# Kernel tuning notes

Measured on AMD Instinct MI355X. Metric: run time of the kernel, lower is better.

The kernel has to match this reference:

```python
import jax, jax.numpy as jnp
import numpy as np

N = 100000   # nodes
E = 1_600_000  # edges (avg degree 16)
D = 64       # input_dim = hidden_dim = output_dim
EPS = 1e-5   # BatchNorm eps


def setup_inputs() -> dict:
    key = jax.random.key(0)
    ks = jax.random.split(key, 8)
    x = jax.random.normal(ks[0], (N, D), jnp.float32)
    edge_index = jax.random.randint(ks[1], (2, E), 0, N, jnp.int32)

    def lin_w(k, din, dout):
        s = 1.0 / np.sqrt(din)
        return jax.random.uniform(k, (din, dout), jnp.float32, -s, s)

    return {
        "x": x, "edge_index": edge_index,
        "W1": lin_w(ks[2], D, D), "b1": jnp.zeros((D,), jnp.float32),
        "g1": jnp.ones((D,), jnp.float32), "be1": jnp.zeros((D,), jnp.float32),
        "W2": lin_w(ks[3], D, D), "b2": jnp.zeros((D,), jnp.float32),
        "g2": jnp.ones((D,), jnp.float32), "be2": jnp.zeros((D,), jnp.float32),
        "W3": lin_w(ks[4], D, D), "b3": jnp.zeros((D,), jnp.float32),
        "g3": jnp.ones((D,), jnp.float32), "be3": jnp.zeros((D,), jnp.float32),
    }


def gcn_conv(x, src, dst, W, b):
    # GCNConv: out = D^{-1/2}(A+I)D^{-1/2} (x @ W) + b
    n = x.shape[0]
    loops = jnp.arange(n, dtype=src.dtype)
    s = jnp.concatenate([src, loops])  # add self-loops
    d = jnp.concatenate([dst, loops])
    deg = jax.ops.segment_sum(jnp.ones_like(s, jnp.float32), d, num_segments=n)
    dinv = jax.lax.rsqrt(jnp.maximum(deg, 1.0))  # deg >= 1 (self-loops)
    norm = dinv[s] * dinv[d]                     # [E+N]
    xw = x @ W                                   # [N, D]
    msgs = xw[s] * norm[:, None]                 # [E+N, D] gather
    return jax.ops.segment_sum(msgs, d, num_segments=n) + b  # scatter-add


def batch_norm(z, g, be):
    # training-mode BatchNorm1d: batch statistics, biased variance
    mu = jnp.mean(z, axis=0)
    var = jnp.mean(jnp.square(z - mu), axis=0)
    return (z - mu) * jax.lax.rsqrt(var + EPS) * g + be


def reference(x, edge_index, W1, b1, g1, be1, W2, b2, g2, be2, W3, b3, g3, be3):
    src, dst = edge_index[0], edge_index[1]
    z = jax.nn.relu(batch_norm(gcn_conv(x, src, dst, W1, b1), g1, be1))
    z = jax.nn.relu(batch_norm(gcn_conv(z, src, dst, W2, b2), g2, be2))
    z = batch_norm(gcn_conv(z, src, dst, W3, b3), g3, be3)
    # dropout (p=0.1) is identity in eval mode; normalize=False default
    return z
```

## Files before the change

### kernel.cpp

```cpp
#include <hip/hip_runtime.h>

typedef unsigned short ushort_t;
typedef unsigned int uint_t;
typedef float f32x4 __attribute__((ext_vector_type(4)));
typedef short bf16x8 __attribute__((ext_vector_type(8)));

#define NB_AGG 2560
#define BSHIFT 7
#define BROWS 128
#define BCAP 4096
#define NCHUNK 256
#define ZP 72

__device__ __forceinline__ float bf2f_lo(uint_t u) {
    union { uint_t i; float f; } v; v.i = u << 16; return v.f;
}
__device__ __forceinline__ float bf2f_hi(uint_t u) {
    union { uint_t i; float f; } v; v.i = u & 0xffff0000u; return v.f;
}
__device__ __forceinline__ ushort_t f2bf(float f) {
    union { float f; uint_t i; } v; v.f = f;
    uint_t u = v.i;
    uint_t r = (u + 0x7fffu + ((u >> 16) & 1u)) >> 16;
    return (ushort_t)r;
}

__global__ __launch_bounds__(256) void hist2_k(const int* __restrict__ dst,
                                               int* __restrict__ H, int E, int nb) {
    __shared__ int h[1024];
    int b = blockIdx.x, t = threadIdx.x;
    for (int i = t; i < nb; i += 256) h[i] = 0;
    __syncthreads();
    int per = (E + NCHUNK - 1) / NCHUNK;
    int lo = b * per, hi = min(E, lo + per);
    for (int e = lo + t; e < hi; e += 256)
        atomicAdd(&h[dst[e] >> BSHIFT], 1);
    __syncthreads();
    for (int i = t; i < nb; i += 256) H[(size_t)i * NCHUNK + b] = h[i];
}

__global__ __launch_bounds__(256) void scanA_k(const int* __restrict__ v,
                                               int* __restrict__ segsum, int total) {
    int base = blockIdx.x * 1024 + threadIdx.x;
    int s = 0;
#pragma unroll
    for (int i = 0; i < 4; ++i) {
        int idx = base + i * 256;
        if (idx < total) s += v[idx];
    }
    __shared__ int sh[256];
    sh[threadIdx.x] = s;
    __syncthreads();
    for (int off = 128; off > 0; off >>= 1) {
        if (threadIdx.x < off) sh[threadIdx.x] += sh[threadIdx.x + off];
        __syncthreads();
    }
    if (threadIdx.x == 0) segsum[blockIdx.x] = sh[0];
}

__global__ void scanB_k(int* segsum, int nseg) {
    __shared__ int sh[256];
    int t = threadIdx.x;
    int own = (t < nseg) ? segsum[t] : 0;
    sh[t] = own;
    __syncthreads();
    for (int off = 1; off < 256; off <<= 1) {
        int v = (t >= off) ? sh[t - off] : 0;
        __syncthreads();
        sh[t] += v;
        __syncthreads();
    }
    if (t < nseg) segsum[t] = sh[t] - own;
}

__global__ __launch_bounds__(256) void scanC2_k(int* __restrict__ H,
                                                const int* __restrict__ segsum,
                                                int total) {
    int t = threadIdx.x;
    int base = blockIdx.x * 1024 + t * 4;
    int c0 = 0, c1 = 0, c2 = 0, c3 = 0;
    if (base + 0 < total) c0 = H[base + 0];
    if (base + 1 < total) c1 = H[base + 1];
    if (base + 2 < total) c2 = H[base + 2];
    if (base + 3 < total) c3 = H[base + 3];
    int tsum = c0 + c1 + c2 + c3;
    __shared__ int sh[256];
    sh[t] = tsum;
    __syncthreads();
    for (int off = 1; off < 256; off <<= 1) {
        int v = (t >= off) ? sh[t - off] : 0;
        __syncthreads();
        sh[t] += v;
        __syncthreads();
    }
    int excl = segsum[blockIdx.x] + sh[t] - tsum;
    if (base + 0 < total) H[base + 0] = excl;
    if (base + 1 < total) H[base + 1] = excl + c0;
    if (base + 2 < total) H[base + 2] = excl + c0 + c1;
    if (base + 3 < total) H[base + 3] = excl + c0 + c1 + c2;
}

__global__ __launch_bounds__(256) void scat2_k(const int* __restrict__ src,
                                               const int* __restrict__ dst,
                                               const int* __restrict__ H,
                                               int* __restrict__ colA, int E, int nb) {
    __shared__ int cur[1024];
    int b = blockIdx.x, t = threadIdx.x;
    for (int i = t; i < nb; i += 256) cur[i] = H[(size_t)i * NCHUNK + b];
    __syncthreads();
    int per = (E + NCHUNK - 1) / NCHUNK;
    int lo = b * per, hi = min(E, lo + per);
    for (int e = lo + t; e < hi; e += 256) {
        int d = dst[e];
        int bk = d >> BSHIFT;
        int pos = atomicAdd(&cur[bk], 1);
        colA[pos] = (src[e] << BSHIFT) | (d & (BROWS - 1));
    }
}

__global__ __launch_bounds__(256) void build_k(int* __restrict__ colA,
                                               const int* __restrict__ H,
                                               float* __restrict__ dinv,
                                               int* __restrict__ rowp,
                                               int N, int E, int nb) {
    __shared__ int recs[BCAP];
    __shared__ int cnt[BROWS], pfx[BROWS], cur[BROWS];
    int b = blockIdx.x, t = threadIdx.x;
    int base = H[(size_t)b * NCHUNK];
    int next = (b + 1 < nb) ? H[(size_t)(b + 1) * NCHUNK] : E;
    int size = next - base;
    if (size > BCAP) size = BCAP;
    int row0 = b << BSHIFT;

    if (t < BROWS) { cnt[t] = 0; cur[t] = 0; }
    __syncthreads();

    for (int i = t; i < size; i += 256) {
        int r = colA[base + i];
        recs[i] = r;
        atomicAdd(&cnt[r & (BROWS - 1)], 1);
    }
    __syncthreads();

    if (t < BROWS) pfx[t] = cnt[t];
    __syncthreads();
    for (int off = 1; off < BROWS; off <<= 1) {
        int u = 0;
        if (t < BROWS && t >= off) u = pfx[t - off];
        __syncthreads();
        if (t < BROWS) pfx[t] += u;
        __syncthreads();
    }
    if (t < BROWS) {
        int row = row0 + t;
        if (row < N) {
            int ex = pfx[t] - cnt[t];
            rowp[row] = base + ex;
            dinv[row] = rsqrtf((float)cnt[t] + 1.0f);
            if (row == N - 1) rowp[N] = base + pfx[t];
        }
    }
    __syncthreads();

    for (int i = t; i < size; i += 256) {
        int r = recs[i];
        int l = r & (BROWS - 1);
        int pos = base + (pfx[l] - cnt[l]) + atomicAdd(&cur[l], 1);
        colA[pos] = r >> BSHIFT;
    }
}

template <int MODE>
__global__ __launch_bounds__(256) void gemm_k(const float* __restrict__ Zf,
                                              const uint2* __restrict__ Zb,
                                              const float* __restrict__ W,
                                              const float* __restrict__ dinv,
                                              const float* __restrict__ cA,
                                              const float* __restrict__ cC,
                                              ushort_t* __restrict__ XW, int N) {
    __shared__ ushort_t WbT[64 * ZP];
    __shared__ ushort_t Zt[64 * ZP];
    __shared__ ushort_t Ot[4][16 * ZP];
    __shared__ float Al[64], Cl[64], Dl[64];
    int t = threadIdx.x;
    int row0 = blockIdx.x * 64;

    if (t < 64) {
        int r = row0 + t;
        Dl[t] = (r < N) ? dinv[r] : 0.0f;
        if (MODE) { Al[t] = cA[t]; Cl[t] = cC[t]; }
    }
    {
        int col = t & 63, kg = t >> 6;
#pragma unroll
        for (int kk = 0; kk < 16; ++kk) {
            int k = kg * 16 + kk;
            WbT[col * ZP + k] = f2bf(W[k * 64 + col]);
        }
    }
    __syncthreads();

    {
        int r = t >> 2, cg = t & 3;
        int grow = row0 + r;
        bool gv = grow < N;
#pragma unroll
        for (int q = 0; q < 4; ++q) {
            float4 v;
            if (MODE) {
                uint2 p2 = {0, 0};
                if (gv) p2 = Zb[(size_t)grow * 16 + cg * 4 + q];
                v.x = bf2f_lo(p2.x); v.y = bf2f_hi(p2.x);
                v.z = bf2f_lo(p2.y); v.w = bf2f_hi(p2.y);
                int k = cg * 16 + q * 4;
                v.x = fmaxf(Al[k + 0] * v.x + Cl[k + 0], 0.0f);
                v.y = fmaxf(Al[k + 1] * v.y + Cl[k + 1], 0.0f);
                v.z = fmaxf(Al[k + 2] * v.z + Cl[k + 2], 0.0f);
                v.w = fmaxf(Al[k + 3] * v.w + Cl[k + 3], 0.0f);
            } else {
                if (gv) v = *(const float4*)(Zf + (size_t)grow * 64 + cg * 16 + q * 4);
                else { v.x = v.y = v.z = v.w = 0.0f; }
            }
            uint2 p;
            p.x = (uint_t)f2bf(v.x) | ((uint_t)f2bf(v.y) << 16);
            p.y = (uint_t)f2bf(v.z) | ((uint_t)f2bf(v.w) << 16);
            *(uint2*)&Zt[r * ZP + cg * 16 + q * 4] = p;
        }
    }
    __syncthreads();

    int wv = t >> 6, lane = t & 63;
    int mrow = lane & 15;
    int kgrp = lane >> 4;

    f32x4 acc0 = {0, 0, 0, 0}, acc1 = {0, 0, 0, 0};
    f32x4 acc2 = {0, 0, 0, 0}, acc3 = {0, 0, 0, 0};
#pragma unroll
    for (int ks = 0; ks < 2; ++ks) {
        bf16x8 a = *(bf16x8*)&Zt[(wv * 16 + mrow) * ZP + ks * 32 + kgrp * 8];
        bf16x8 b0 = *(bf16x8*)&WbT[(0 + mrow) * ZP + ks * 32 + kgrp * 8];
        bf16x8 b1 = *(bf16x8*)&WbT[(16 + mrow) * ZP + ks * 32 + kgrp * 8];
        bf16x8 b2 = *(bf16x8*)&WbT[(32 + mrow) * ZP + ks * 32 + kgrp * 8];
        bf16x8 b3 = *(bf16x8*)&WbT[(48 + mrow) * ZP + ks * 32 + kgrp * 8];
        acc0 = __builtin_amdgcn_mfma_f32_16x16x32_bf16(a, b0, acc0, 0, 0, 0);
        acc1 = __builtin_amdgcn_mfma_f32_16x16x32_bf16(a, b1, acc1, 0, 0, 0);
        acc2 = __builtin_amdgcn_mfma_f32_16x16x32_bf16(a, b2, acc2, 0, 0, 0);
        acc3 = __builtin_amdgcn_mfma_f32_16x16x32_bf16(a, b3, acc3, 0, 0, 0);
    }

#pragma unroll
    for (int r = 0; r < 4; ++r) {
        int orow = kgrp * 4 + r;
        float dn = Dl[wv * 16 + orow];
        Ot[wv][orow * ZP + 0 + mrow]  = f2bf(acc0[r] * dn);
        Ot[wv][orow * ZP + 16 + mrow] = f2bf(acc1[r] * dn);
        Ot[wv][orow * ZP + 32 + mrow] = f2bf(acc2[r] * dn);
        Ot[wv][orow * ZP + 48 + mrow] = f2bf(acc3[r] * dn);
    }
#pragma unroll
    for (int i = 0; i < 2; ++i) {
        int cid = lane * 2 + i;
        int orow = cid >> 3, seg = cid & 7;
        int grow = row0 + wv * 16 + orow;
        if (grow < N)
            *(uint4*)(XW + (size_t)grow * 64 + seg * 8) =
                *(uint4*)&Ot[wv][orow * ZP + seg * 8];
    }
}

template <int WBF16>
__global__ __launch_bounds__(256) void agg_k(const ushort_t* __restrict__ y,
                                             const int* __restrict__ row_ptr,
                                             const int* __restrict__ colA,
                                             const float* __restrict__ dinv,
                                             float* __restrict__ OUTF,
                                             uint2* __restrict__ OUTB,
                                             float* __restrict__ pS,
                                             float* __restrict__ pQ, int N) {
    __shared__ float ssum[64], ssq[64];
    int t = threadIdx.x, lane = t & 63, wv = t >> 6;
    int rs = lane >> 5;
    int g = (lane >> 4) & 1;
    int c = lane & 15;
    if (t < 64) ssum[t] = 0.0f;
    else if (t < 128) ssq[t - 64] = 0.0f;
    __syncthreads();

    const uint2* y2 = (const uint2*)y;
    float ps0 = 0, ps1 = 0, ps2 = 0, ps3 = 0;
    float pq0 = 0, pq1 = 0, pq2 = 0, pq3 = 0;

    int npair = (N + 1) >> 1;
    for (int p = blockIdx.x * 4 + wv; p < npair; p += NB_AGG * 4) {
        int row = p * 2 + rs;
        bool rv = row < N;
        int rc = rv ? row : N - 1;
        int start = row_ptr[rc];
        int end = row_ptr[rc + 1];
        int len = rv ? (end - start) : 0;
        int ml = max(len, __shfl_xor(len, 32));

        float a0 = 0, a1 = 0, a2 = 0, a3 = 0;
        for (int off = 0; off < ml; off += 16) {
            int sA[8];
            uint_t mA[8];
#pragma unroll
            for (int u = 0; u < 8; ++u) {
                int slot = off + u * 2 + g;
                bool val = slot < len;
                int ec = val ? (start + slot) : 0;
                sA[u] = colA[ec];
                mA[u] = val ? 0xffffffffu : 0u;
            }
#pragma unroll
            for (int u = 0; u < 8; ++u) {
                uint2 v = y2[(size_t)sA[u] * 16 + c];
                v.x &= mA[u]; v.y &= mA[u];
                a0 += bf2f_lo(v.x);
                a1 += bf2f_hi(v.x);
                a2 += bf2f_lo(v.y);
                a3 += bf2f_hi(v.y);
            }
        }

        a0 += __shfl_xor(a0, 16);
        a1 += __shfl_xor(a1, 16);
        a2 += __shfl_xor(a2, 16);
        a3 += __shfl_xor(a3, 16);

        if (g == 0 && rv) {
            float dn = dinv[row];
            uint2 sv = y2[(size_t)row * 16 + c];
            float v0 = dn * (a0 + bf2f_lo(sv.x));
            float v1 = dn * (a1 + bf2f_hi(sv.x));
            float v2 = dn * (a2 + bf2f_lo(sv.y));
            float v3 = dn * (a3 + bf2f_hi(sv.y));
            if (WBF16) {
                uint2 pk;
                pk.x = (uint_t)f2bf(v0) | ((uint_t)f2bf(v1) << 16);
                pk.y = (uint_t)f2bf(v2) | ((uint_t)f2bf(v3) << 16);
                OUTB[(size_t)row * 16 + c] = pk;
            } else {
                float4 o; o.x = v0; o.y = v1; o.z = v2; o.w = v3;
                *(float4*)(OUTF + (size_t)row * 64 + c * 4) = o;
            }
            ps0 += v0; ps1 += v1; ps2 += v2; ps3 += v3;
            pq0 += v0 * v0; pq1 += v1 * v1; pq2 += v2 * v2; pq3 += v3 * v3;
        }
    }

    if (g == 0) {
        atomicAdd(&ssum[c * 4 + 0], ps0); atomicAdd(&ssq[c * 4 + 0], pq0);
        atomicAdd(&ssum[c * 4 + 1], ps1); atomicAdd(&ssq[c * 4 + 1], pq1);
        atomicAdd(&ssum[c * 4 + 2], ps2); atomicAdd(&ssq[c * 4 + 2], pq2);
        atomicAdd(&ssum[c * 4 + 3], ps3); atomicAdd(&ssq[c * 4 + 3], pq3);
    }
    __syncthreads();
    if (t < 64) pS[(size_t)t * NB_AGG + blockIdx.x] = ssum[t];
    else if (t < 128) pQ[(size_t)(t - 64) * NB_AGG + blockIdx.x] = ssq[t - 64];
}

__global__ __launch_bounds__(256) void stats_k(const float* __restrict__ pS,
                                               const float* __restrict__ pQ,
                                               const float* __restrict__ g,
                                               const float* __restrict__ be,
                                               float* __restrict__ cA,
                                               float* __restrict__ cC, int N) {
    int c = blockIdx.x, t = threadIdx.x;
    float s = 0.0f, q = 0.0f;
    for (int i = t; i < NB_AGG; i += 256) {
        s += pS[(size_t)c * NB_AGG + i];
        q += pQ[(size_t)c * NB_AGG + i];
    }
    __shared__ float rs[256], rq[256];
    rs[t] = s; rq[t] = q;
    __syncthreads();
    for (int off = 128; off > 0; off >>= 1) {
        if (t < off) { rs[t] += rs[t + off]; rq[t] += rq[t + off]; }
        __syncthreads();
    }
    if (t == 0) {
        float mu = rs[0] / (float)N;
        float var = rq[0] / (float)N - mu * mu;
        var = fmaxf(var, 0.0f);
        float inv = rsqrtf(var + 1e-5f);
        float a = g[c] * inv;
        cA[c] = a;
        cC[c] = be[c] - mu * a;
    }
}

__global__ __launch_bounds__(256) void apply_k(float* __restrict__ O,
                                               const float* __restrict__ cA,
                                               const float* __restrict__ cC,
                                               int N) {
    int total = N * 16;
    for (int i = blockIdx.x * 256 + threadIdx.x; i < total; i += gridDim.x * 256) {
        float4 v = ((float4*)O)[i];
        int c = (i & 15) * 4;
        v.x = cA[c + 0] * v.x + cC[c + 0];
        v.y = cA[c + 1] * v.y + cC[c + 1];
        v.z = cA[c + 2] * v.z + cC[c + 2];
        v.w = cA[c + 3] * v.w + cC[c + 3];
        ((float4*)O)[i] = v;
    }
}

extern "C" void kernel_launch(void* const* d_in, const int* in_sizes, int n_in,
                              void* d_out, int out_size, void* d_ws, size_t ws_size,
                              hipStream_t stream) {
    const float* x   = (const float*)d_in[0];
    const int*   ei  = (const int*)d_in[1];
    const float* W1  = (const float*)d_in[2];
    const float* g1  = (const float*)d_in[4];
    const float* be1 = (const float*)d_in[5];
    const float* W2  = (const float*)d_in[6];
    const float* g2  = (const float*)d_in[8];
    const float* be2 = (const float*)d_in[9];
    const float* W3  = (const float*)d_in[10];
    const float* g3  = (const float*)d_in[12];
    const float* be3 = (const float*)d_in[13];

    int N = in_sizes[0] / 64;
    int E = in_sizes[1] / 2;
    const int* srcA = ei;
    const int* dstA = ei + E;
    int nb = (N + BROWS - 1) >> BSHIFT;
    int total = nb * NCHUNK;
    int nseg = (total + 1023) / 1024;

    char* w = (char*)d_ws;
    auto alloc = [&](size_t bytes) -> char* {
        char* p = w;
        w += (bytes + 255) & ~(size_t)255;
        return p;
    };
    ushort_t* xw    = (ushort_t*)alloc((size_t)N * 64 * 2);
    uint2*    zb    = (uint2*)alloc((size_t)N * 64 * 2);
    int*      rowp  = (int*)alloc(((size_t)N + 1) * 4);
    float*    dinv  = (float*)alloc((size_t)N * 4);
    int*      colA  = (int*)alloc((size_t)E * 4);
    int*      H     = (int*)alloc((size_t)total * 4);
    int*      segsum= (int*)alloc((size_t)nseg * 4);
    float*    pS    = (float*)alloc((size_t)64 * NB_AGG * 4);
    float*    pQ    = (float*)alloc((size_t)64 * NB_AGG * 4);
    float*    cA1 = (float*)alloc(256); float* cC1 = (float*)alloc(256);
    float*    cA2 = (float*)alloc(256); float* cC2 = (float*)alloc(256);
    float*    cA3 = (float*)alloc(256); float* cC3 = (float*)alloc(256);
    (void)ws_size; (void)n_in; (void)out_size;

    float* out = (float*)d_out;

    hist2_k<<<NCHUNK, 256, 0, stream>>>(dstA, H, E, nb);
    scanA_k<<<nseg, 256, 0, stream>>>(H, segsum, total);
    scanB_k<<<1, 256, 0, stream>>>(segsum, nseg);
    scanC2_k<<<nseg, 256, 0, stream>>>(H, segsum, total);
    scat2_k<<<NCHUNK, 256, 0, stream>>>(srcA, dstA, H, colA, E, nb);
    build_k<<<nb, 256, 0, stream>>>(colA, H, dinv, rowp, N, E, nb);

    int gemmGrid = (N + 63) / 64;

    gemm_k<0><<<gemmGrid, 256, 0, stream>>>(x, nullptr, W1, dinv, nullptr, nullptr, xw, N);
    agg_k<1><<<NB_AGG, 256, 0, stream>>>(xw, rowp, colA, dinv, nullptr, zb, pS, pQ, N);
    stats_k<<<64, 256, 0, stream>>>(pS, pQ, g1, be1, cA1, cC1, N);

    gemm_k<1><<<gemmGrid, 256, 0, stream>>>(nullptr, zb, W2, dinv, cA1, cC1, xw, N);
    agg_k<1><<<NB_AGG, 256, 0, stream>>>(xw, rowp, colA, dinv, nullptr, zb, pS, pQ, N);
    stats_k<<<64, 256, 0, stream>>>(pS, pQ, g2, be2, cA2, cC2, N);

    gemm_k<1><<<gemmGrid, 256, 0, stream>>>(nullptr, zb, W3, dinv, cA2, cC2, xw, N);
    agg_k<0><<<NB_AGG, 256, 0, stream>>>(xw, rowp, colA, dinv, out, nullptr, pS, pQ, N);
    stats_k<<<64, 256, 0, stream>>>(pS, pQ, g3, be3, cA3, cC3, N);

    apply_k<<<2048, 256, 0, stream>>>(out, cA3, cC3, N);
}
```

Measured before the change: 245.3 us.

## Aggregate four rows per wavefront and store final layer in bf16

The aggregation kernel now gives each 16-lane group its own row, so a wavefront handles four rows and the cross-half shuffle reduction goes away. Each row walks its own neighbour list eight edges at a time instead of two groups interleaving edges. The final layer also writes bf16 intermediates, and the apply kernel turns them back into float output, cutting the fp32 write and read-modify-write traffic. The cost is lower precision on the final output, and more lane divergence when rows in the same wavefront have different degrees.

```diff
diff --git a/kernel.cpp b/kernel.cpp
--- a/kernel.cpp
+++ b/kernel.cpp
@@ -268,19 +268,15 @@
     }
 }
 
-template <int WBF16>
 __global__ __launch_bounds__(256) void agg_k(const ushort_t* __restrict__ y,
                                              const int* __restrict__ row_ptr,
                                              const int* __restrict__ colA,
                                              const float* __restrict__ dinv,
-                                             float* __restrict__ OUTF,
                                              uint2* __restrict__ OUTB,
                                              float* __restrict__ pS,
                                              float* __restrict__ pQ, int N) {
     __shared__ float ssum[64], ssq[64];
     int t = threadIdx.x, lane = t & 63, wv = t >> 6;
-    int rs = lane >> 5;
-    int g = (lane >> 4) & 1;
     int c = lane & 15;
     if (t < 64) ssum[t] = 0.0f;
     else if (t < 128) ssq[t - 64] = 0.0f;
@@ -290,23 +286,23 @@
     float ps0 = 0, ps1 = 0, ps2 = 0, ps3 = 0;
     float pq0 = 0, pq1 = 0, pq2 = 0, pq3 = 0;
 
-    int npair = (N + 1) >> 1;
-    for (int p = blockIdx.x * 4 + wv; p < npair; p += NB_AGG * 4) {
-        int row = p * 2 + rs;
+    int nquad = (N + 3) >> 2;
+    for (int q = blockIdx.x * 4 + wv; q < nquad; q += NB_AGG * 4) {
+        int row = q * 4 + (lane >> 4);
         bool rv = row < N;
         int rc = rv ? row : N - 1;
         int start = row_ptr[rc];
         int end = row_ptr[rc + 1];
         int len = rv ? (end - start) : 0;
-        int ml = max(len, __shfl_xor(len, 32));
+        float dn = rv ? dinv[row] : 0.0f;
 
         float a0 = 0, a1 = 0, a2 = 0, a3 = 0;
-        for (int off = 0; off < ml; off += 16) {
+        for (int off = 0; off < len; off += 8) {
             int sA[8];
             uint_t mA[8];
 #pragma unroll
             for (int u = 0; u < 8; ++u) {
-                int slot = off + u * 2 + g;
+                int slot = off + u;
                 bool val = slot < len;
                 int ec = val ? (start + slot) : 0;
                 sA[u] = colA[ec];
@@ -323,38 +319,25 @@
             }
         }
 
-        a0 += __shfl_xor(a0, 16);
-        a1 += __shfl_xor(a1, 16);
-        a2 += __shfl_xor(a2, 16);
-        a3 += __shfl_xor(a3, 16);
-
-        if (g == 0 && rv) {
-            float dn = dinv[row];
+        if (rv) {
             uint2 sv = y2[(size_t)row * 16 + c];
             float v0 = dn * (a0 + bf2f_lo(sv.x));
             float v1 = dn * (a1 + bf2f_hi(sv.x));
             float v2 = dn * (a2 + bf2f_lo(sv.y));
             float v3 = dn * (a3 + bf2f_hi(sv.y));
-            if (WBF16) {
-                uint2 pk;
-                pk.x = (uint_t)f2bf(v0) | ((uint_t)f2bf(v1) << 16);
-                pk.y = (uint_t)f2bf(v2) | ((uint_t)f2bf(v3) << 16);
-                OUTB[(size_t)row * 16 + c] = pk;
-            } else {
-                float4 o; o.x = v0; o.y = v1; o.z = v2; o.w = v3;
-                *(float4*)(OUTF + (size_t)row * 64 + c * 4) = o;
-            }
+            uint2 pk;
+            pk.x = (uint_t)f2bf(v0) | ((uint_t)f2bf(v1) << 16);
+            pk.y = (uint_t)f2bf(v2) | ((uint_t)f2bf(v3) << 16);
+            OUTB[(size_t)row * 16 + c] = pk;
             ps0 += v0; ps1 += v1; ps2 += v2; ps3 += v3;
             pq0 += v0 * v0; pq1 += v1 * v1; pq2 += v2 * v2; pq3 += v3 * v3;
         }
     }
 
-    if (g == 0) {
-        atomicAdd(&ssum[c * 4 + 0], ps0); atomicAdd(&ssq[c * 4 + 0], pq0);
-        atomicAdd(&ssum[c * 4 + 1], ps1); atomicAdd(&ssq[c * 4 + 1], pq1);
-        atomicAdd(&ssum[c * 4 + 2], ps2); atomicAdd(&ssq[c * 4 + 2], pq2);
-        atomicAdd(&ssum[c * 4 + 3], ps3); atomicAdd(&ssq[c * 4 + 3], pq3);
-    }
+    atomicAdd(&ssum[c * 4 + 0], ps0); atomicAdd(&ssq[c * 4 + 0], pq0);
+    atomicAdd(&ssum[c * 4 + 1], ps1); atomicAdd(&ssq[c * 4 + 1], pq1);
+    atomicAdd(&ssum[c * 4 + 2], ps2); atomicAdd(&ssq[c * 4 + 2], pq2);
+    atomicAdd(&ssum[c * 4 + 3], ps3); atomicAdd(&ssq[c * 4 + 3], pq3);
     __syncthreads();
     if (t < 64) pS[(size_t)t * NB_AGG + blockIdx.x] = ssum[t];
     else if (t < 128) pQ[(size_t)(t - 64) * NB_AGG + blockIdx.x] = ssq[t - 64];
@@ -390,18 +373,20 @@
     }
 }
 
-__global__ __launch_bounds__(256) void apply_k(float* __restrict__ O,
+__global__ __launch_bounds__(256) void apply_k(const uint2* __restrict__ Zb,
+                                               float* __restrict__ O,
                                                const float* __restrict__ cA,
                                                const float* __restrict__ cC,
                                                int N) {
     int total = N * 16;
     for (int i = blockIdx.x * 256 + threadIdx.x; i < total; i += gridDim.x * 256) {
-        float4 v = ((float4*)O)[i];
+        uint2 p = Zb[i];
         int c = (i & 15) * 4;
-        v.x = cA[c + 0] * v.x + cC[c + 0];
-        v.y = cA[c + 1] * v.y + cC[c + 1];
-        v.z = cA[c + 2] * v.z + cC[c + 2];
-        v.w = cA[c + 3] * v.w + cC[c + 3];
+        float4 v;
+        v.x = cA[c + 0] * bf2f_lo(p.x) + cC[c + 0];
+        v.y = cA[c + 1] * bf2f_hi(p.x) + cC[c + 1];
+        v.z = cA[c + 2] * bf2f_lo(p.y) + cC[c + 2];
+        v.w = cA[c + 3] * bf2f_hi(p.y) + cC[c + 3];
         ((float4*)O)[i] = v;
     }
 }
@@ -461,16 +446,16 @@
     int gemmGrid = (N + 63) / 64;
 
     gemm_k<0><<<gemmGrid, 256, 0, stream>>>(x, nullptr, W1, dinv, nullptr, nullptr, xw, N);
-    agg_k<1><<<NB_AGG, 256, 0, stream>>>(xw, rowp, colA, dinv, nullptr, zb, pS, pQ, N);
+    agg_k<<<NB_AGG, 256, 0, stream>>>(xw, rowp, colA, dinv, zb, pS, pQ, N);
     stats_k<<<64, 256, 0, stream>>>(pS, pQ, g1, be1, cA1, cC1, N);
 
     gemm_k<1><<<gemmGrid, 256, 0, stream>>>(nullptr, zb, W2, dinv, cA1, cC1, xw, N);
-    agg_k<1><<<NB_AGG, 256, 0, stream>>>(xw, rowp, colA, dinv, nullptr, zb, pS, pQ, N);
+    agg_k<<<NB_AGG, 256, 0, stream>>>(xw, rowp, colA, dinv, zb, pS, pQ, N);
     stats_k<<<64, 256, 0, stream>>>(pS, pQ, g2, be2, cA2, cC2, N);
 
     gemm_k<1><<<gemmGrid, 256, 0, stream>>>(nullptr, zb, W3, dinv, cA2, cC2, xw, N);
-    agg_k<0><<<NB_AGG, 256, 0, stream>>>(xw, rowp, colA, dinv, out, nullptr, pS, pQ, N);
+    agg_k<<<NB_AGG, 256, 0, stream>>>(xw, rowp, colA, dinv, zb, pS, pQ, N);
     stats_k<<<64, 256, 0, stream>>>(pS, pQ, g3, be3, cA3, cC3, N);
 
-    apply_k<<<2048, 256, 0, stream>>>(out, cA3, cC3, N);
-}
+    apply_k<<<2048, 256, 0, stream>>>(zb, out, cA3, cC3, N);
+}
```

Result: slower. 274.6 us (+11.9%).
